# Kernel optimization log

Hardware: AMD Instinct MI355X
Metric: run time of the kernel (lower is better)

## Reference

```python
import jax, jax.numpy as jnp
import numpy as np

COMMITMENT_COST = 0.25
NUM_EMBEDDINGS = 1024
EMB_DIMS = [64, 128, 256]
RES = [(96, 320), (48, 160), (24, 80)]
BATCH = 8


def setup_inputs() -> dict:
    key = jax.random.key(0)
    ks = jax.random.split(key, 6)
    inp = {}
    for i, (d, (h, w)) in enumerate(zip(EMB_DIMS, RES)):
        inp[f"x{i}"] = jax.random.normal(ks[i], (BATCH, d, h, w), dtype=jnp.float32)
        inp[f"emb{i}"] = jax.random.normal(ks[3 + i], (NUM_EMBEDDINGS, d), dtype=jnp.float32)
    return inp


def _quantize_level(x, emb):
    # x: [B, D, H, W], emb: [K, D]
    B, D, H, W = x.shape
    xf = jnp.transpose(x, (0, 2, 3, 1)).reshape(-1, D)  # [N, D]
    dist = (
        jnp.sum(xf * xf, axis=1, keepdims=True)
        + jnp.sum(emb * emb, axis=1)
        - 2.0 * xf @ emb.T
    )
    idx = jnp.argmin(dist, axis=1)  # [N]
    q = emb[idx]  # gather == one-hot @ emb in the original
    # commitment loss (quantized is detached in e_latent_loss)
    loss = COMMITMENT_COST * jnp.mean((jax.lax.stop_gradient(q) - xf) ** 2)
    # straight-through estimator
    q_st = xf + jax.lax.stop_gradient(q - xf)
    q_out = jnp.transpose(q_st.reshape(B, H, W, D), (0, 3, 1, 2))  # back to NCHW
    return loss, q_out


def reference(x0, x1, x2, emb0, emb1, emb2):
    # eval-mode MultiCodebook.forward (return_indices=False, return_features=False)
    total_loss = jnp.float32(0.0)
    feats = []
    for x, emb in ((x0, emb0), (x1, emb1), (x2, emb2)):
        loss, q = _quantize_level(x, emb)
        total_loss = total_loss + loss
        feats.append(q)
    return (total_loss, feats[0], feats[1], feats[2])
```

## Files before the change

kernel.cpp:

```cpp
#include <hip/hip_runtime.h>
#include <float.h>

typedef __bf16 bf16x8 __attribute__((ext_vector_type(8)));
typedef float  f32x16 __attribute__((ext_vector_type(16)));

#define WS_EE    0
#define WS_SLOT  12288
#define WS_IMG0  16384
#define WS_IMG1  (WS_IMG0 + 4096 * 64)
#define WS_IMG2  (WS_IMG1 + 4096 * 128)

__device__ __forceinline__ short f2bf(float f) {
    unsigned u = __float_as_uint(f);
    unsigned r = (u + 0x7FFFu + ((u >> 16) & 1u)) >> 16;
    return (short)r;
}
__device__ __forceinline__ float bf2f(short s) {
    return __uint_as_float(((unsigned)(unsigned short)s) << 16);
}
__device__ __forceinline__ unsigned pk2(short a, short b) {
    return (unsigned)(unsigned short)a | ((unsigned)(unsigned short)b << 16);
}

__device__ __forceinline__ void stage_tile(const char* __restrict__ src, short* dst, int tid)
{
    const char* s = src + tid * 16;
    char* d = (char*)dst + tid * 16;
#pragma unroll
    for (int it = 0; it < 8; ++it) {
        __builtin_amdgcn_global_load_lds(
            (const __attribute__((address_space(1))) void*)(s + it * 4096),
            (__attribute__((address_space(3))) void*)(d + it * 4096),
            16, 0, 0);
    }
}

__global__ void prep_all(const float* __restrict__ e0, const float* __restrict__ e1,
                         const float* __restrict__ e2, char* __restrict__ ws)
{
    int bid = blockIdx.x;
    if (bid >= 224) {
        int b2 = bid - 224;
        float* ee = (float*)ws;
        const float* e; float* o; int D;
        if (b2 < 256)      { e = e0; o = ee;        D = 64;  }
        else if (b2 < 512) { e = e1; o = ee + 1024; D = 128; b2 -= 256; }
        else               { e = e2; o = ee + 2048; D = 256; b2 -= 512; }
        int k  = b2 * 4 + (threadIdx.x >> 6);
        int ln = threadIdx.x & 63;
        float s = 0.f;
        for (int d = ln; d < D; d += 64) { float v = e[(size_t)k * D + d]; s = fmaf(v, v, s); }
#pragma unroll
        for (int m = 32; m >= 1; m >>= 1) s += __shfl_xor(s, m);
        if (ln == 0) o[k] = s;
        return;
    }
    int flat = bid * 256 + threadIdx.x;
    const float* emb; char* img; int D, id;
    if (flat < 8192)       { emb = e0; img = ws + WS_IMG0; D = 64;  id = flat; }
    else if (flat < 24576) { emb = e1; img = ws + WS_IMG1; D = 128; id = flat - 8192; }
    else                   { emb = e2; img = ws + WS_IMG2; D = 256; id = flat - 24576; }
    int chunks = D >> 3;
    int c  = id / chunks;
    int ch = id - c * chunks;
    int d0 = ch * 8;
    int kc = d0 >> 6;
    int dd = d0 & 63;
    int q  = ((dd >> 4) << 2) + (((dd >> 3) & 1) << 1);
    int r  = c & 127;
    int ct = c >> 7;
    const float* s = emb + (size_t)c * D + d0;
    unsigned hw[4], lw[4];
#pragma unroll
    for (int j = 0; j < 4; ++j) {
        float va = s[2 * j], vb = s[2 * j + 1];
        short ha = f2bf(va), hb = f2bf(vb);
        short la = f2bf(va - bf2f(ha)), lb = f2bf(vb - bf2f(hb));
        hw[j] = pk2(ha, hb);
        lw[j] = pk2(la, lb);
    }
    char* base = img + ((size_t)(ct * (D >> 6) + kc)) * 32768 + r * 256;
    *(uint4*)(base + (((q    ) ^ (r & 15)) << 4)) = make_uint4(hw[0], hw[1], hw[2], hw[3]);
    *(uint4*)(base + (((q + 1) ^ (r & 15)) << 4)) = make_uint4(lw[0], lw[1], lw[2], lw[3]);
}

__shared__ __align__(16) short g_eb0[16384];
__shared__ __align__(16) short g_eb1[16384];
__shared__ __align__(16) float g_ee[1024];
__shared__ float g_m1[128];
__shared__ float g_m2[128];
__shared__ int   g_i1[128];
__shared__ int   g_sidx[128];
__shared__ float g_d1[128];
__shared__ int   g_flag[130];
__shared__ unsigned long long g_red;
__shared__ float g_part[4];

template<int D, int HW, int PTS>
__device__ void vq_core3(const float* __restrict__ x, const float* __restrict__ emb,
                         const float* __restrict__ eesq, const char* __restrict__ eimg,
                         float* __restrict__ feat, float* __restrict__ slots,
                         float lscale, float margin, int ptblk)
{
    constexpr int KCS  = D / 64;
    constexpr int ROWG = PTS / 32;
    constexpr int TPW  = ROWG;
    constexpr int W    = 4 / ROWG;
    constexpr int NT   = 8 * KCS;
    constexpr bool SA  = (TPW <= 2);

    const int tid  = threadIdx.x;
    const int L    = tid & 63;
    const int wave = tid >> 6;
    const int col  = L & 31;
    const int half = L >> 5;
    const int rowg = wave % ROWG;
    const int cgrp = wave / ROWG;

    const int pt0 = ptblk * PTS;
    const int b   = pt0 / HW;
    const int hw0 = pt0 % HW;
    const float* xb = x + (size_t)b * D * HW + hw0;

    stage_tile(eimg, g_eb1, tid);

    short* gx = g_eb0;
    float ssq = 0.f;
#pragma unroll
    for (int it = 0; it < 4; ++it) {
        int flat = it * 256 + tid;
        int pt   = flat % PTS;
        int dch  = flat / PTS;
        int d0   = dch * 8;
        int kc   = d0 >> 6;
        int dd   = d0 & 63;
        int q    = ((dd >> 4) << 2) + (((dd >> 3) & 1) << 1);
        unsigned hw_[4], lw_[4];
#pragma unroll
        for (int j = 0; j < 4; ++j) {
            float va = xb[(size_t)(d0 + 2 * j)     * HW + pt];
            float vb = xb[(size_t)(d0 + 2 * j + 1) * HW + pt];
            ssq = fmaf(va, va, ssq);
            ssq = fmaf(vb, vb, ssq);
            short ha = f2bf(va), hb = f2bf(vb);
            short la = f2bf(va - bf2f(ha)), lb = f2bf(vb - bf2f(hb));
            hw_[j] = pk2(ha, hb);
            lw_[j] = pk2(la, lb);
        }
        short* row = gx + kc * (PTS * 128) + pt * 128;
        *(uint4*)(row + (((q    ) ^ (pt & 15)) << 3)) = make_uint4(hw_[0], hw_[1], hw_[2], hw_[3]);
        *(uint4*)(row + (((q + 1) ^ (pt & 15)) << 3)) = make_uint4(lw_[0], lw_[1], lw_[2], lw_[3]);
    }
#pragma unroll
    for (int i = 0; i < 4; ++i) g_ee[i * 256 + tid] = eesq[i * 256 + tid];
    if (tid == 0) g_flag[0] = 0;

    asm volatile("s_waitcnt lgkmcnt(0)" ::: "memory");
    __builtin_amdgcn_s_barrier();
    __builtin_amdgcn_sched_barrier(0);

    const int arow = rowg * 32 + col;
    const short* xrow0 = gx + arow * 128;
    bf16x8 afh[KCS][4], afl[KCS][4];
#pragma unroll
    for (int kc = 0; kc < KCS; ++kc) {
        const short* xck = xrow0 + kc * (PTS * 128);
#pragma unroll
        for (int t4 = 0; t4 < 4; ++t4) {
            int qh = t4 * 4 + half * 2;
            afh[kc][t4] = *(const bf16x8*)(xck + (((qh    ) ^ (arow & 15)) << 3));
            afl[kc][t4] = *(const bf16x8*)(xck + (((qh + 1) ^ (arow & 15)) << 3));
        }
    }
    asm volatile("s_waitcnt lgkmcnt(0)" ::: "memory");
    __builtin_amdgcn_s_barrier();
    __builtin_amdgcn_sched_barrier(0);
    stage_tile(eimg + 32768, g_eb0, tid);

    float m1[16], m2[16]; int i1[16];
#pragma unroll
    for (int r = 0; r < 16; ++r) { m1[r] = FLT_MAX; m2[r] = FLT_MAX; i1[r] = 0; }

    for (int cg = 0; cg < 8; ++cg) {
        float eecv[TPW];
#pragma unroll
        for (int tt = 0; tt < TPW; ++tt)
            eecv[tt] = g_ee[cg * 128 + (cgrp * TPW + tt) * 32 + col];

        f32x16 acc[TPW];
        f32x16 acc2[SA ? TPW : 1];
#pragma unroll
        for (int tt = 0; tt < TPW; ++tt)
#pragma unroll
            for (int j = 0; j < 16; ++j) acc[tt][j] = 0.f;
        if constexpr (SA) {
#pragma unroll
            for (int tt = 0; tt < TPW; ++tt)
#pragma unroll
                for (int j = 0; j < 16; ++j) acc2[tt][j] = 0.f;
        }

#pragma unroll
        for (int kc = 0; kc < KCS; ++kc) {
            const int t = cg * KCS + kc;
            short* buft = (t & 1) ? g_eb0 : g_eb1;
            if (t == NT - 1) asm volatile("s_waitcnt vmcnt(0)" ::: "memory");
            else             asm volatile("s_waitcnt vmcnt(8)" ::: "memory");
            __builtin_amdgcn_s_barrier();
            __builtin_amdgcn_sched_barrier(0);
#pragma unroll
            for (int t4 = 0; t4 < 4; ++t4) {
                const int qh = t4 * 4 + half * 2;
#pragma unroll
                for (int tt = 0; tt < TPW; ++tt) {
                    const int brow = (cgrp * TPW + tt) * 32 + col;
                    const short* br = buft + brow * 128;
                    bf16x8 bh = *(const bf16x8*)(br + (((qh    ) ^ (brow & 15)) << 3));
                    bf16x8 bl = *(const bf16x8*)(br + (((qh + 1) ^ (brow & 15)) << 3));
                    if constexpr (SA) {
                        acc [tt] = __builtin_amdgcn_mfma_f32_32x32x16_bf16(afh[kc][t4], bh, acc [tt], 0, 0, 0);
                        acc2[tt] = __builtin_amdgcn_mfma_f32_32x32x16_bf16(afh[kc][t4], bl, acc2[tt], 0, 0, 0);
                        acc2[tt] = __builtin_amdgcn_mfma_f32_32x32x16_bf16(afl[kc][t4], bh, acc2[tt], 0, 0, 0);
                    } else {
                        acc[tt] = __builtin_amdgcn_mfma_f32_32x32x16_bf16(afh[kc][t4], bh, acc[tt], 0, 0, 0);
                        acc[tt] = __builtin_amdgcn_mfma_f32_32x32x16_bf16(afh[kc][t4], bl, acc[tt], 0, 0, 0);
                        acc[tt] = __builtin_amdgcn_mfma_f32_32x32x16_bf16(afl[kc][t4], bh, acc[tt], 0, 0, 0);
                    }
                }
            }
            asm volatile("s_waitcnt lgkmcnt(0)" ::: "memory");
            __builtin_amdgcn_s_barrier();
            __builtin_amdgcn_sched_barrier(0);
            if (t + 2 < NT) stage_tile(eimg + (size_t)(t + 2) * 32768, buft, tid);
        }

#pragma unroll
        for (int tt = 0; tt < TPW; ++tt) {
            int c = cg * 128 + (cgrp * TPW + tt) * 32 + col;
            float eec = eecv[tt];
#pragma unroll
            for (int r = 0; r < 16; ++r) {
                float av = acc[tt][r];
                if constexpr (SA) av += acc2[tt][r];
                float dist = fmaf(-2.f, av, eec);
                m2[r] = __builtin_amdgcn_fmed3f(dist, m1[r], m2[r]);
                bool lt = dist < m1[r];
                m1[r] = lt ? dist : m1[r];
                i1[r] = lt ? c : i1[r];
            }
        }
    }

#pragma unroll
    for (int r = 0; r < 16; ++r) {
#pragma unroll
        for (int msk = 1; msk <= 16; msk <<= 1) {
            float om1 = __shfl_xor(m1[r], msk);
            int   oi  = __shfl_xor(i1[r], msk);
            float om2 = __shfl_xor(m2[r], msk);
            float mx  = fmaxf(m1[r], om1);
            m2[r] = fminf(mx, fminf(m2[r], om2));
            bool tk = (om1 < m1[r]) || (om1 == m1[r] && oi < i1[r]);
            m1[r] = tk ? om1 : m1[r];
            i1[r] = tk ? oi  : i1[r];
        }
    }
#pragma unroll
    for (int r = 0; r < 16; ++r) {
        int r16 = (r & 3) + 8 * (r >> 2) + 4 * half;
        if (col == r16) {
            int p = rowg * 32 + r16;
            g_m1[p * W + cgrp] = m1[r];
            g_m2[p * W + cgrp] = m2[r];
            g_i1[p * W + cgrp] = i1[r];
        }
    }
    __syncthreads();

    if (tid < PTS) {
        float bm1 = FLT_MAX, bm2 = FLT_MAX; int bi = 0x7FFFFFFF;
#pragma unroll
        for (int s = 0; s < W; ++s) {
            float am1 = g_m1[tid * W + s];
            float am2 = g_m2[tid * W + s];
            int   ai  = g_i1[tid * W + s];
            float mx  = fmaxf(bm1, am1);
            bm2 = fminf(mx, fminf(bm2, am2));
            bool tk = (am1 < bm1) || (am1 == bm1 && ai < bi);
            bm1 = tk ? am1 : bm1;
            bi  = tk ? ai  : bi;
        }
        g_sidx[tid] = bi;
        g_d1[tid]   = bm1;
        if (bm2 - bm1 <= margin) {
            int pos = atomicAdd(&g_flag[0], 1);
            g_flag[1 + pos] = tid;
        }
    }
    __syncthreads();

    int nf = g_flag[0];
    float* sx = (float*)g_eb0;
    for (int i = 0; i < nf; ++i) {
        int p   = g_flag[1 + i];
        int phw = hw0 + p;
        for (int d = tid; d < D; d += 256) sx[d] = x[((size_t)b * D + d) * HW + phw];
        if (tid == 0) g_red = ~0ull;
        __syncthreads();
#pragma unroll
        for (int j = 0; j < 4; ++j) {
            int c = j * 256 + tid;
            float s = 0.f;
#pragma unroll 4
            for (int d = 0; d < D; ++d) s = fmaf(sx[d], emb[(size_t)c * D + d], s);
            float dist = fmaf(-2.f, s, g_ee[c]);
            unsigned u = __float_as_uint(dist);
            u = (u >> 31) ? ~u : (u | 0x80000000u);
            unsigned long long pkv = ((unsigned long long)u << 32) | (unsigned)c;
            atomicMin(&g_red, pkv);
        }
        __syncthreads();
        if (tid == 0) {
            unsigned u = (unsigned)(g_red >> 32);
            unsigned orig = (u & 0x80000000u) ? (u ^ 0x80000000u) : ~u;
            g_sidx[p] = (int)(g_red & 0xFFFFFFFFu);
            g_d1[p]   = __uint_as_float(orig);
        }
        __syncthreads();
    }

#pragma unroll 4
    for (int it = 0; it < (PTS * D) / 256; ++it) {
        int flat = it * 256 + tid;
        int p  = flat % PTS;
        int dd = flat / PTS;
        int k  = g_sidx[p];
        feat[((size_t)b * D + dd) * HW + hw0 + p] = emb[(size_t)k * D + dd];
    }

    float lsum = ssq;
    if (tid < PTS) lsum += g_d1[tid];
#pragma unroll
    for (int m = 32; m >= 1; m >>= 1) lsum += __shfl_xor(lsum, m);
    if (L == 0) g_part[wave] = lsum;
    __syncthreads();
    if (tid == 0) {
        float tot = (g_part[0] + g_part[1]) + (g_part[2] + g_part[3]);
        atomicAdd(&slots[blockIdx.x & 127], tot * lscale);
    }
}

__global__ __launch_bounds__(256, 2)
void vq_main3(const float* __restrict__ x0, const float* __restrict__ e0,
              const float* __restrict__ x1, const float* __restrict__ e1,
              const float* __restrict__ x2, const float* __restrict__ e2,
              char* __restrict__ ws,
              float* __restrict__ f0, float* __restrict__ f1, float* __restrict__ f2)
{
    const float* ee = (const float*)ws;
    float* slots = (float*)(ws + WS_SLOT);
    int bid = blockIdx.x;
    if (bid < 480) {
        vq_core3<256, 1920, 32>(x2, e2, ee + 2048, ws + WS_IMG2, f2, slots,
                                0.25f / 3932160.f, 8e-3f, bid);
    } else if (bid < 1440) {
        vq_core3<128, 7680, 64>(x1, e1, ee + 1024, ws + WS_IMG1, f1, slots,
                                0.25f / 7864320.f, 5e-3f, bid - 480);
    } else {
        vq_core3<64, 30720, 128>(x0, e0, ee, ws + WS_IMG0, f0, slots,
                                 0.25f / 15728640.f, 4e-3f, bid - 1440);
    }
}

__global__ void loss_finish(const float* __restrict__ slots, float* __restrict__ out)
{
    int t = threadIdx.x;
    float v = slots[t];
#pragma unroll
    for (int m = 32; m >= 1; m >>= 1) v += __shfl_xor(v, m);
    __shared__ float p2[2];
    if ((t & 63) == 0) p2[t >> 6] = v;
    __syncthreads();
    if (t == 0) out[0] = p2[0] + p2[1];
}

extern "C" void kernel_launch(void* const* d_in, const int* in_sizes, int n_in,
                              void* d_out, int out_size, void* d_ws, size_t ws_size,
                              hipStream_t stream)
{
    const float* x0 = (const float*)d_in[0];
    const float* e0 = (const float*)d_in[1];
    const float* x1 = (const float*)d_in[2];
    const float* e1 = (const float*)d_in[3];
    const float* x2 = (const float*)d_in[4];
    const float* e2 = (const float*)d_in[5];

    float* out  = (float*)d_out;
    float* f0   = out + 1;
    float* f1   = f0 + 15728640;
    float* f2   = f1 + 7864320;

    char* ws = (char*)d_ws;
    float* slots = (float*)(ws + WS_SLOT);

    hipMemsetAsync(slots, 0, 128 * sizeof(float), stream);

    prep_all<<<992, 256, 0, stream>>>(e0, e1, e2, ws);

    vq_main3<<<3360, 256, 0, stream>>>(x0, e0, x1, e1, x2, e2, ws, f0, f1, f2);

    loss_finish<<<1, 128, 0, stream>>>(slots, out);
}
```

Baseline: 522.0 us.

## Read codebook MFMA operands directly from global memory instead of LDS double-buffering

Drops the LDS double-buffered staging of the bf16 hi/lo codebook tiles. The prep kernel now writes the image in a lane-contiguous layout, so each MFMA B operand is loaded straight from global memory (L2-resident) with coalesced 16-byte loads. The x operand is now read from LDS per k-chunk instead of being held in registers, and launch bounds are raised to 3 blocks per CU, since LDS use falls from about 64KB to about 32KB. The aim is to remove the per-tile barriers and LDS staging overhead and gain occupancy, at the risk of exposed global/L2 load latency in the inner MFMA loop.

```diff
diff --git a/kernel.cpp b/kernel.cpp
--- a/kernel.cpp
+++ b/kernel.cpp
@@ -20,19 +20,6 @@
 }
 __device__ __forceinline__ unsigned pk2(short a, short b) {
     return (unsigned)(unsigned short)a | ((unsigned)(unsigned short)b << 16);
-}
-
-__device__ __forceinline__ void stage_tile(const char* __restrict__ src, short* dst, int tid)
-{
-    const char* s = src + tid * 16;
-    char* d = (char*)dst + tid * 16;
-#pragma unroll
-    for (int it = 0; it < 8; ++it) {
-        __builtin_amdgcn_global_load_lds(
-            (const __attribute__((address_space(1))) void*)(s + it * 4096),
-            (__attribute__((address_space(3))) void*)(d + it * 4096),
-            16, 0, 0);
-    }
 }
 
 __global__ void prep_all(const float* __restrict__ e0, const float* __restrict__ e1,
@@ -79,14 +66,14 @@
         hw[j] = pk2(ha, hb);
         lw[j] = pk2(la, lb);
     }
-    char* base = img + ((size_t)(ct * (D >> 6) + kc)) * 32768 + r * 256;
-    *(uint4*)(base + (((q    ) ^ (r & 15)) << 4)) = make_uint4(hw[0], hw[1], hw[2], hw[3]);
-    *(uint4*)(base + (((q + 1) ^ (r & 15)) << 4)) = make_uint4(lw[0], lw[1], lw[2], lw[3]);
-}
-
-__shared__ __align__(16) short g_eb0[16384];
-__shared__ __align__(16) short g_eb1[16384];
+    char* base = img + ((size_t)(ct * (D >> 6) + kc)) * 32768 + r * 16;
+    *(uint4*)(base + ((q    ) << 11)) = make_uint4(hw[0], hw[1], hw[2], hw[3]);
+    *(uint4*)(base + ((q + 1) << 11)) = make_uint4(lw[0], lw[1], lw[2], lw[3]);
+}
+
+__shared__ __align__(16) short g_x[16384];
 __shared__ __align__(16) float g_ee[1024];
+__shared__ __align__(16) float g_sx[256];
 __shared__ float g_m1[128];
 __shared__ float g_m2[128];
 __shared__ int   g_i1[128];
@@ -97,7 +84,7 @@
 __shared__ float g_part[4];
 
 template<int D, int HW, int PTS>
-__device__ void vq_core3(const float* __restrict__ x, const float* __restrict__ emb,
+__device__ void vq_core4(const float* __restrict__ x, const float* __restrict__ emb,
                          const float* __restrict__ eesq, const char* __restrict__ eimg,
                          float* __restrict__ feat, float* __restrict__ slots,
                          float lscale, float margin, int ptblk)
@@ -106,7 +93,6 @@
     constexpr int ROWG = PTS / 32;
     constexpr int TPW  = ROWG;
     constexpr int W    = 4 / ROWG;
-    constexpr int NT   = 8 * KCS;
     constexpr bool SA  = (TPW <= 2);
 
     const int tid  = threadIdx.x;
@@ -122,9 +108,6 @@
     const int hw0 = pt0 % HW;
     const float* xb = x + (size_t)b * D * HW + hw0;
 
-    stage_tile(eimg, g_eb1, tid);
-
-    short* gx = g_eb0;
     float ssq = 0.f;
 #pragma unroll
     for (int it = 0; it < 4; ++it) {
@@ -147,39 +130,22 @@
             hw_[j] = pk2(ha, hb);
             lw_[j] = pk2(la, lb);
         }
-        short* row = gx + kc * (PTS * 128) + pt * 128;
+        short* row = g_x + kc * (PTS * 128) + pt * 128;
         *(uint4*)(row + (((q    ) ^ (pt & 15)) << 3)) = make_uint4(hw_[0], hw_[1], hw_[2], hw_[3]);
         *(uint4*)(row + (((q + 1) ^ (pt & 15)) << 3)) = make_uint4(lw_[0], lw_[1], lw_[2], lw_[3]);
     }
 #pragma unroll
     for (int i = 0; i < 4; ++i) g_ee[i * 256 + tid] = eesq[i * 256 + tid];
     if (tid == 0) g_flag[0] = 0;
-
-    asm volatile("s_waitcnt lgkmcnt(0)" ::: "memory");
-    __builtin_amdgcn_s_barrier();
-    __builtin_amdgcn_sched_barrier(0);
+    __syncthreads();
+
+    float m1[16], m2[16]; int i1[16];
+#pragma unroll
+    for (int r = 0; r < 16; ++r) { m1[r] = FLT_MAX; m2[r] = FLT_MAX; i1[r] = 0; }
 
     const int arow = rowg * 32 + col;
-    const short* xrow0 = gx + arow * 128;
-    bf16x8 afh[KCS][4], afl[KCS][4];
-#pragma unroll
-    for (int kc = 0; kc < KCS; ++kc) {
-        const short* xck = xrow0 + kc * (PTS * 128);
-#pragma unroll
-        for (int t4 = 0; t4 < 4; ++t4) {
-            int qh = t4 * 4 + half * 2;
-            afh[kc][t4] = *(const bf16x8*)(xck + (((qh    ) ^ (arow & 15)) << 3));
-            afl[kc][t4] = *(const bf16x8*)(xck + (((qh + 1) ^ (arow & 15)) << 3));
-        }
-    }
-    asm volatile("s_waitcnt lgkmcnt(0)" ::: "memory");
-    __builtin_amdgcn_s_barrier();
-    __builtin_amdgcn_sched_barrier(0);
-    stage_tile(eimg + 32768, g_eb0, tid);
-
-    float m1[16], m2[16]; int i1[16];
-#pragma unroll
-    for (int r = 0; r < 16; ++r) { m1[r] = FLT_MAX; m2[r] = FLT_MAX; i1[r] = 0; }
+    const short* xrow0 = g_x + arow * 128;
+    const int boff_lane = (half << 12) + (col << 4);
 
     for (int cg = 0; cg < 8; ++cg) {
         float eecv[TPW];
@@ -200,38 +166,33 @@
                 for (int j = 0; j < 16; ++j) acc2[tt][j] = 0.f;
         }
 
+        const char* tb = eimg + (size_t)cg * (KCS * 32768);
 #pragma unroll
         for (int kc = 0; kc < KCS; ++kc) {
-            const int t = cg * KCS + kc;
-            short* buft = (t & 1) ? g_eb0 : g_eb1;
-            if (t == NT - 1) asm volatile("s_waitcnt vmcnt(0)" ::: "memory");
-            else             asm volatile("s_waitcnt vmcnt(8)" ::: "memory");
-            __builtin_amdgcn_s_barrier();
-            __builtin_amdgcn_sched_barrier(0);
+            const short* xck = xrow0 + kc * (PTS * 128);
+            const char* tbk = tb + kc * 32768;
 #pragma unroll
             for (int t4 = 0; t4 < 4; ++t4) {
                 const int qh = t4 * 4 + half * 2;
+                bf16x8 ah = *(const bf16x8*)(xck + (((qh    ) ^ (arow & 15)) << 3));
+                bf16x8 al = *(const bf16x8*)(xck + (((qh + 1) ^ (arow & 15)) << 3));
+                const char* tq = tbk + (t4 << 13) + boff_lane;
 #pragma unroll
                 for (int tt = 0; tt < TPW; ++tt) {
-                    const int brow = (cgrp * TPW + tt) * 32 + col;
-                    const short* br = buft + brow * 128;
-                    bf16x8 bh = *(const bf16x8*)(br + (((qh    ) ^ (brow & 15)) << 3));
-                    bf16x8 bl = *(const bf16x8*)(br + (((qh + 1) ^ (brow & 15)) << 3));
+                    const char* bp = tq + ((cgrp * TPW + tt) << 9);
+                    bf16x8 bh = *(const bf16x8*)(bp);
+                    bf16x8 bl = *(const bf16x8*)(bp + 2048);
                     if constexpr (SA) {
-                        acc [tt] = __builtin_amdgcn_mfma_f32_32x32x16_bf16(afh[kc][t4], bh, acc [tt], 0, 0, 0);
-                        acc2[tt] = __builtin_amdgcn_mfma_f32_32x32x16_bf16(afh[kc][t4], bl, acc2[tt], 0, 0, 0);
-                        acc2[tt] = __builtin_amdgcn_mfma_f32_32x32x16_bf16(afl[kc][t4], bh, acc2[tt], 0, 0, 0);
+                        acc [tt] = __builtin_amdgcn_mfma_f32_32x32x16_bf16(ah, bh, acc [tt], 0, 0, 0);
+                        acc2[tt] = __builtin_amdgcn_mfma_f32_32x32x16_bf16(ah, bl, acc2[tt], 0, 0, 0);
+                        acc2[tt] = __builtin_amdgcn_mfma_f32_32x32x16_bf16(al, bh, acc2[tt], 0, 0, 0);
                     } else {
-                        acc[tt] = __builtin_amdgcn_mfma_f32_32x32x16_bf16(afh[kc][t4], bh, acc[tt], 0, 0, 0);
-                        acc[tt] = __builtin_amdgcn_mfma_f32_32x32x16_bf16(afh[kc][t4], bl, acc[tt], 0, 0, 0);
-                        acc[tt] = __builtin_amdgcn_mfma_f32_32x32x16_bf16(afl[kc][t4], bh, acc[tt], 0, 0, 0);
+                        acc[tt] = __builtin_amdgcn_mfma_f32_32x32x16_bf16(ah, bh, acc[tt], 0, 0, 0);
+                        acc[tt] = __builtin_amdgcn_mfma_f32_32x32x16_bf16(ah, bl, acc[tt], 0, 0, 0);
+                        acc[tt] = __builtin_amdgcn_mfma_f32_32x32x16_bf16(al, bh, acc[tt], 0, 0, 0);
                     }
                 }
             }
-            asm volatile("s_waitcnt lgkmcnt(0)" ::: "memory");
-            __builtin_amdgcn_s_barrier();
-            __builtin_amdgcn_sched_barrier(0);
-            if (t + 2 < NT) stage_tile(eimg + (size_t)(t + 2) * 32768, buft, tid);
         }
 
 #pragma unroll
@@ -300,11 +261,10 @@
     __syncthreads();
 
     int nf = g_flag[0];
-    float* sx = (float*)g_eb0;
     for (int i = 0; i < nf; ++i) {
         int p   = g_flag[1 + i];
         int phw = hw0 + p;
-        for (int d = tid; d < D; d += 256) sx[d] = x[((size_t)b * D + d) * HW + phw];
+        for (int d = tid; d < D; d += 256) g_sx[d] = x[((size_t)b * D + d) * HW + phw];
         if (tid == 0) g_red = ~0ull;
         __syncthreads();
 #pragma unroll
@@ -312,7 +272,7 @@
             int c = j * 256 + tid;
             float s = 0.f;
 #pragma unroll 4
-            for (int d = 0; d < D; ++d) s = fmaf(sx[d], emb[(size_t)c * D + d], s);
+            for (int d = 0; d < D; ++d) s = fmaf(g_sx[d], emb[(size_t)c * D + d], s);
             float dist = fmaf(-2.f, s, g_ee[c]);
             unsigned u = __float_as_uint(dist);
             u = (u >> 31) ? ~u : (u | 0x80000000u);
@@ -350,8 +310,8 @@
     }
 }
 
-__global__ __launch_bounds__(256, 2)
-void vq_main3(const float* __restrict__ x0, const float* __restrict__ e0,
+__global__ __launch_bounds__(256, 3)
+void vq_main4(const float* __restrict__ x0, const float* __restrict__ e0,
               const float* __restrict__ x1, const float* __restrict__ e1,
               const float* __restrict__ x2, const float* __restrict__ e2,
               char* __restrict__ ws,
@@ -361,13 +321,13 @@
     float* slots = (float*)(ws + WS_SLOT);
     int bid = blockIdx.x;
     if (bid < 480) {
-        vq_core3<256, 1920, 32>(x2, e2, ee + 2048, ws + WS_IMG2, f2, slots,
+        vq_core4<256, 1920, 32>(x2, e2, ee + 2048, ws + WS_IMG2, f2, slots,
                                 0.25f / 3932160.f, 8e-3f, bid);
     } else if (bid < 1440) {
-        vq_core3<128, 7680, 64>(x1, e1, ee + 1024, ws + WS_IMG1, f1, slots,
+        vq_core4<128, 7680, 64>(x1, e1, ee + 1024, ws + WS_IMG1, f1, slots,
                                 0.25f / 7864320.f, 5e-3f, bid - 480);
     } else {
-        vq_core3<64, 30720, 128>(x0, e0, ee, ws + WS_IMG0, f0, slots,
+        vq_core4<64, 30720, 128>(x0, e0, ee, ws + WS_IMG0, f0, slots,
                                  0.25f / 15728640.f, 4e-3f, bid - 1440);
     }
 }
@@ -407,7 +367,7 @@
 
     prep_all<<<992, 256, 0, stream>>>(e0, e1, e2, ws);
 
-    vq_main3<<<3360, 256, 0, stream>>>(x0, e0, x1, e1, x2, e2, ws, f0, f1, f2);
+    vq_main4<<<3360, 256, 0, stream>>>(x0, e0, x1, e1, x2, e2, ws, f0, f1, f2);
 
     loss_finish<<<1, 128, 0, stream>>>(slots, out);
 }
```

Result: slower. 603.0 us (+15.5%).
